# Performance work log

Hardware: AMD Instinct MI355X
Metric: run time of the kernel (lower is better)

Reference implementation:

```python
import jax, jax.numpy as jnp
import numpy as np

N, E, H = 50000, 800000, 4
IN, HID, OUT = 128, 64, 16
SIM_THRESH = 0.1
NEG_SLOPE = 0.01  # F.leaky_relu default


def setup_inputs() -> dict:
    key = jax.random.key(0)
    k = jax.random.split(key, 6)
    x = jax.random.normal(k[0], (N, IN), jnp.float32)
    row = jax.random.randint(k[1], (E,), 0, N)
    col = jax.random.randint(k[2], (E,), 0, N)
    W0 = jax.random.normal(k[3], (H, IN, HID), jnp.float32) / np.float32(np.sqrt(IN))
    W1 = jax.random.normal(k[4], (H, H * HID, HID), jnp.float32) / np.float32(np.sqrt(H * HID))
    W2 = jax.random.normal(k[5], (1, H * HID, OUT), jnp.float32) / np.float32(np.sqrt(H * HID))
    return {"x": x, "W0": W0, "W1": W1, "W2": W2, "row": row, "col": col}


def _att_coef(x, row, col):
    # cosine similarity on edges only (honors the sparse edge structure)
    nrm = jnp.linalg.norm(x, axis=1, keepdims=True)
    xn = x / jnp.maximum(nrm, 1e-12)
    sim = jnp.sum(xn[row] * xn[col], axis=1)            # [E]
    sim = jnp.where(sim < SIM_THRESH, 0.0, sim)
    # L1 row-normalize the thresholded attention matrix
    rowsum = jax.ops.segment_sum(jnp.abs(sim), row, num_segments=N)
    rs_e = rowsum[row]
    att = jnp.where(rs_e > 0, sim / jnp.where(rs_e > 0, rs_e, 1.0), 0.0)
    # degree-based self-loop weight lam = 1/(deg+1), then exp of all nonzeros
    deg = jax.ops.segment_sum((att != 0).astype(x.dtype), row, num_segments=N)
    w_edge = jnp.where(att != 0, jnp.exp(att), 0.0)     # zero entries stay zero (dropped nnz)
    w_self = jnp.exp(1.0 / (deg + 1.0))                 # [N]
    return w_edge, w_self


def _layer(x, W, row, col, act):
    w_edge, w_self = _att_coef(x, row, col)
    z = jnp.einsum('nd,hdo->nho', x, W)                 # per-head projection
    msg = w_edge[:, None, None] * z[col]                # [E,h,o] gather + weight
    agg = jax.ops.segment_sum(msg, row, num_segments=N) + w_self[:, None, None] * z
    out = agg.reshape(N, -1)                            # concat heads (flatten(1))
    return jax.nn.leaky_relu(out, NEG_SLOPE) if act else out


def reference(x, W0, W1, W2, row, col):
    h = _layer(x, W0, row, col, True)
    h = _layer(h, W1, row, col, True)
    h = _layer(h, W2, row, col, False)
    return h
```

## Files before the change

kernel.cpp:

```cpp
#include <hip/hip_runtime.h>
#include <math.h>


static inline int cdiv(int a, int b){ return (a + b - 1) / b; }


__device__ inline float vdot(float4 a, float4 b){ return a.x*b.x + a.y*b.y + a.z*b.z + a.w*b.w; }
__device__ inline void vfma(float4& acc, float w, float4 b){
  acc.x += w*b.x; acc.y += w*b.y; acc.z += w*b.z; acc.w += w*b.w;
}
__device__ inline float4 vscale(float w, float4 a){ return make_float4(w*a.x, w*a.y, w*a.z, w*a.w); }

__device__ inline float wred(float d){
  #pragma unroll
  for (int off = 32; off; off >>= 1) d += __shfl_xor(d, off);
  return d;
}

__device__ inline unsigned short f2bf(float f){
  unsigned int u = __float_as_uint(f);
  unsigned int r = (u + 0x7FFFu + ((u >> 16) & 1u)) >> 16;
  return (unsigned short)r;
}
__device__ inline float bf2f(unsigned int us){ return __uint_as_float(us << 16); }

__device__ inline void bf8_to_f(uint4 v, float* f){
  f[0] = bf2f(v.x & 0xFFFFu); f[1] = bf2f(v.x >> 16);
  f[2] = bf2f(v.y & 0xFFFFu); f[3] = bf2f(v.y >> 16);
  f[4] = bf2f(v.z & 0xFFFFu); f[5] = bf2f(v.z >> 16);
  f[6] = bf2f(v.w & 0xFFFFu); f[7] = bf2f(v.w >> 16);
}

typedef __attribute__((ext_vector_type(8))) short bf16x8;
typedef __attribute__((ext_vector_type(4))) float f32x4;


__global__ void count_kernel(const int* __restrict__ row, int* __restrict__ cnt, int E){
  int e = blockIdx.x * blockDim.x + threadIdx.x;
  if (e < E) atomicAdd(&cnt[row[e]], 1);
}

__global__ void scan1_kernel(const int* __restrict__ cnt, int* __restrict__ offs,
                             int* __restrict__ bsum, int n){
  __shared__ int tmp[256];
  int tid = threadIdx.x;
  int g = blockIdx.x * 256 + tid;
  int v = (g < n) ? cnt[g] : 0;
  tmp[tid] = v;
  __syncthreads();
  for (int off = 1; off < 256; off <<= 1){
    int t = (tid >= off) ? tmp[tid - off] : 0;
    __syncthreads();
    tmp[tid] += t;
    __syncthreads();
  }
  if (g < n) offs[g] = tmp[tid] - v;
  if (tid == 255) bsum[blockIdx.x] = tmp[255];
}

__global__ void scan2_kernel(int* __restrict__ bsum, int* __restrict__ offs, int nb, int n){
  __shared__ int tmp[256];
  int tid = threadIdx.x;
  int v = (tid < nb) ? bsum[tid] : 0;
  tmp[tid] = v;
  __syncthreads();
  for (int off = 1; off < 256; off <<= 1){
    int t = (tid >= off) ? tmp[tid - off] : 0;
    __syncthreads();
    tmp[tid] += t;
    __syncthreads();
  }
  if (tid < nb) bsum[tid] = tmp[tid] - v;
  if (tid == 255) offs[n] = tmp[255];
}

__global__ void scan3_kernel(int* __restrict__ offs, int* __restrict__ cur,
                             const int* __restrict__ bsum, int n){
  int g = blockIdx.x * 256 + threadIdx.x;
  if (g < n){
    int o = offs[g] + bsum[blockIdx.x];
    offs[g] = o;
    cur[g]  = o;
  }
}

__global__ void scatter_kernel(const int* __restrict__ row, const int* __restrict__ col,
                               int* __restrict__ cur, int* __restrict__ ecol, int E){
  int e = blockIdx.x * blockDim.x + threadIdx.x;
  if (e < E){
    int p = atomicAdd(&cur[row[e]], 1);
    ecol[p] = col[e];
  }
}


__global__ void invnorm128_kernel(const float* __restrict__ x, float* __restrict__ invn, int N){
  int n = blockIdx.x * 4 + (threadIdx.x >> 6);
  int lane = threadIdx.x & 63;
  if (n >= N) return;
  float2 a = ((const float2*)(x + (size_t)n * 128))[lane];
  float ss = a.x * a.x + a.y * a.y;
  ss = wred(ss);
  if (lane == 0) invn[n] = 1.0f / fmaxf(sqrtf(ss), 1e-12f);
}


template<int R>
__global__ void att_agg_wave128(const float* __restrict__ x, const float* __restrict__ invn,
                                const int* __restrict__ offs, const int* __restrict__ ecol,
                                float* __restrict__ out, int N){
  constexpr int LT = 64;
  __shared__ float tls[4][LT];
  __shared__ int   tlk[4][LT];
  const int wid  = threadIdx.x >> 6;
  const int lane = threadIdx.x & 63;
  const int half = lane >> 5, hl = lane & 31;
  const int hidx = wid * 2 + half;
  const int n = blockIdx.x * 2 + wid;
  if (n >= N) return;
  const int s = offs[n], e = offs[n + 1];
  const float inr = invn[n];
  const float4* xv = (const float4*)x;
  float4 a = xv[(size_t)n * 32 + hl];

  float4 br[R];
  float  simv[R];
  float  rowsum = 0.0f;
  int    deg = 0;

  #pragma unroll
  for (int r = 0; r < R; r++){
    simv[r] = 0.0f;
    int k = s + 2 * r + half;
    if (k < e){
      int c = ecol[k];
      float4 b = xv[(size_t)c * 32 + hl];
      br[r] = b;
      float d = vdot(a, b);
      #pragma unroll
      for (int off = 16; off; off >>= 1) d += __shfl_xor(d, off);
      d *= inr * invn[c];
      if (d < 0.1f) d = 0.0f;
      simv[r] = d;
      rowsum += d;
      deg += (d != 0.0f) ? 1 : 0;
    }
  }

  int tc = 0, kover = e;
  int k = s + 2 * R + half;
  for (; k + 2 < e; k += 4){
    int c0 = ecol[k], c1 = ecol[k + 2];
    float4 b0 = xv[(size_t)c0 * 32 + hl];
    float4 b1 = xv[(size_t)c1 * 32 + hl];
    float d0 = vdot(a, b0), d1 = vdot(a, b1);
    #pragma unroll
    for (int off = 16; off; off >>= 1){ d0 += __shfl_xor(d0, off); d1 += __shfl_xor(d1, off); }
    d0 *= inr * invn[c0];
    d1 *= inr * invn[c1];
    if (d0 < 0.1f) d0 = 0.0f;
    if (d1 < 0.1f) d1 = 0.0f;
    rowsum += d0 + d1;
    deg += (d0 != 0.0f) + (d1 != 0.0f);
    if (d0 > 0.0f){
      if (tc < LT){ if (hl == 0){ tls[hidx][tc] = d0; tlk[hidx][tc] = c0; } tc++; }
      else if (kover > k) kover = k;
    }
    if (d1 > 0.0f){
      if (tc < LT){ if (hl == 0){ tls[hidx][tc] = d1; tlk[hidx][tc] = c1; } tc++; }
      else if (kover > k + 2) kover = k + 2;
    }
  }
  if (k < e){
    int c0 = ecol[k];
    float4 b0 = xv[(size_t)c0 * 32 + hl];
    float d0 = vdot(a, b0);
    #pragma unroll
    for (int off = 16; off; off >>= 1) d0 += __shfl_xor(d0, off);
    d0 *= inr * invn[c0];
    if (d0 < 0.1f) d0 = 0.0f;
    rowsum += d0;
    deg += (d0 != 0.0f) ? 1 : 0;
    if (d0 > 0.0f){
      if (tc < LT){ if (hl == 0){ tls[hidx][tc] = d0; tlk[hidx][tc] = c0; } tc++; }
      else if (kover > k) kover = k;
    }
  }

  rowsum += __shfl_xor(rowsum, 32);
  deg    += __shfl_xor(deg, 32);
  const float invrs = (rowsum > 0.0f) ? 1.0f / rowsum : 0.0f;
  const float wself = expf(1.0f / (float)(deg + 1));

  float4 acc = (half == 0) ? vscale(wself, a) : make_float4(0.f, 0.f, 0.f, 0.f);
  #pragma unroll
  for (int r = 0; r < R; r++){
    if (simv[r] > 0.0f) vfma(acc, expf(simv[r] * invrs), br[r]);
  }
  int j = 0;
  for (; j + 1 < tc; j += 2){
    float w0 = expf(tls[hidx][j] * invrs);
    float w1 = expf(tls[hidx][j + 1] * invrs);
    int c0 = tlk[hidx][j], c1 = tlk[hidx][j + 1];
    float4 b0 = xv[(size_t)c0 * 32 + hl];
    float4 b1 = xv[(size_t)c1 * 32 + hl];
    vfma(acc, w0, b0);
    vfma(acc, w1, b1);
  }
  if (j < tc){
    float w0 = expf(tls[hidx][j] * invrs);
    float4 b0 = xv[(size_t)tlk[hidx][j] * 32 + hl];
    vfma(acc, w0, b0);
  }
  for (int k2 = kover; k2 < e; k2 += 2){
    int c = ecol[k2];
    float4 b = xv[(size_t)c * 32 + hl];
    float d = vdot(a, b);
    #pragma unroll
    for (int off = 16; off; off >>= 1) d += __shfl_xor(d, off);
    d *= inr * invn[c];
    if (d >= 0.1f) vfma(acc, expf(d * invrs), b);
  }

  acc.x += __shfl_xor(acc.x, 32);
  acc.y += __shfl_xor(acc.y, 32);
  acc.z += __shfl_xor(acc.z, 32);
  acc.w += __shfl_xor(acc.w, 32);
  if (half == 0) ((float4*)out)[(size_t)n * 32 + hl] = acc;
}


template<int LT>
__device__ inline void sim_rows_mfma(const uint4* __restrict__ hb4,
                                     const float* __restrict__ invn,
                                     const int* __restrict__ ecol,
                                     uint4* __restrict__ tile,
                                     int n, int s, int e, float inr,
                                     float* __restrict__ tls, int* __restrict__ tlk,
                                     float& rowsum_o, int& deg_o, int& tcl_o, int& kover_o){
  const int l = threadIdx.x & 63;
  const int g = l >> 4;
  const int m = l & 15;
  const int lr = l & 31;
  const int rh = l >> 5;
  const bf16x8* hbv = (const bf16x8*)hb4;

  bf16x8 bfrag[8];
  #pragma unroll
  for (int f = 0; f < 8; f++) bfrag[f] = hbv[(size_t)n * 32 + f * 4 + g];

  float rowsum = 0.0f;
  int deg = 0, tc = 0, kover = e;

  for (int k0 = s; k0 < e; k0 += 16){
    int idx = k0 + m;
    int kk = (idx < e) ? idx : (e - 1);
    int c_l = ecol[kk];
    float ic_l = invn[c_l];

    #pragma unroll
    for (int f = 0; f < 8; f++){
      int rsel = 2 * f + rh;
      int crow = __shfl(c_l, rsel);
      tile[(size_t)lr * 17 + rsel] = hb4[(size_t)crow * 32 + lr];
    }

    f32x4 acc0 = {0.f, 0.f, 0.f, 0.f};
    f32x4 acc1 = {0.f, 0.f, 0.f, 0.f};
    #pragma unroll
    for (int f = 0; f < 8; f += 2){
      bf16x8 av0 = *(const bf16x8*)&tile[(size_t)(g + 4 * f) * 17 + m];
      bf16x8 av1 = *(const bf16x8*)&tile[(size_t)(g + 4 * (f + 1)) * 17 + m];
      acc0 = __builtin_amdgcn_mfma_f32_16x16x32_bf16(av0, bfrag[f],     acc0, 0, 0, 0);
      acc1 = __builtin_amdgcn_mfma_f32_16x16x32_bf16(av1, bfrag[f + 1], acc1, 0, 0, 0);
    }

    float dv[4]; int cm[4];
    int bits = 0;
    #pragma unroll
    for (int r = 0; r < 4; r++){
      int mm = g * 4 + r;
      cm[r] = __shfl(c_l, mm);
      float ic = __shfl(ic_l, mm);
      float d = (acc0[r] + acc1[r]) * inr * ic;
      if (d < 0.1f || (k0 + mm) >= e) d = 0.0f;
      dv[r] = d;
      rowsum += d;
      deg += (d != 0.0f) ? 1 : 0;
      if (d > 0.0f) bits |= (1 << r);
    }
    int M16 = bits << (g * 4);
    M16 |= __shfl_xor(M16, 16);
    M16 |= __shfl_xor(M16, 32);
    #pragma unroll
    for (int r = 0; r < 4; r++){
      if (m == 0 && dv[r] > 0.0f){
        int mm = g * 4 + r;
        int pos = tc + __popc(M16 & ((1 << mm) - 1));
        if (pos < LT){ tls[pos] = dv[r]; tlk[pos] = cm[r]; }
        else if (k0 + mm < kover) kover = k0 + mm;
      }
    }
    tc += __popc(M16);
  }
  rowsum += __shfl_xor(rowsum, 16);
  rowsum += __shfl_xor(rowsum, 32);
  deg    += __shfl_xor(deg, 16);
  deg    += __shfl_xor(deg, 32);
  #pragma unroll
  for (int off = 32; off; off >>= 1) kover = min(kover, __shfl_xor(kover, off));
  rowsum_o = rowsum; deg_o = deg;
  tcl_o = (tc < LT) ? tc : LT;
  kover_o = kover;
}


template<int LT>
__global__ __launch_bounds__(128) void att256_mfma(
    const unsigned short* __restrict__ hbf, const float* __restrict__ invn,
    const int* __restrict__ offs, const int* __restrict__ ecol,
    float* __restrict__ out, int N){
  __shared__ float tls[2][LT];
  __shared__ int   tlk[2][LT];
  __shared__ uint4 tile[2][32 * 17];
  const int wid = threadIdx.x >> 6;
  const int l   = threadIdx.x & 63;
  const int n = blockIdx.x * 2 + wid;
  if (n >= N) return;
  const int s = offs[n], e = offs[n + 1];
  const float inr = invn[n];
  const uint4* hb4 = (const uint4*)hbf;

  float rowsum; int deg, tcl, kover;
  sim_rows_mfma<LT>(hb4, invn, ecol, tile[wid], n, s, e, inr, tls[wid], tlk[wid],
                    rowsum, deg, tcl, kover);

  const float invrs = (rowsum > 0.0f) ? 1.0f / rowsum : 0.0f;
  const float wself = expf(1.0f / (float)(deg + 1));

  const int half = l >> 5, hl = l & 31;
  float a8[8]; bf8_to_f(hb4[(size_t)n * 32 + hl], a8);
  float acc8[8];
  #pragma unroll
  for (int t = 0; t < 8; t++) acc8[t] = (half == 0) ? wself * a8[t] : 0.0f;

  int j = half;
  for (; j + 2 < tcl; j += 4){
    float w0 = expf(tls[wid][j] * invrs);
    float w1 = expf(tls[wid][j + 2] * invrs);
    uint4 v0 = hb4[(size_t)tlk[wid][j] * 32 + hl];
    uint4 v1 = hb4[(size_t)tlk[wid][j + 2] * 32 + hl];
    float b0[8], b1[8];
    bf8_to_f(v0, b0); bf8_to_f(v1, b1);
    #pragma unroll
    for (int t = 0; t < 8; t++) acc8[t] += w0 * b0[t] + w1 * b1[t];
  }
  if (j < tcl){
    float w0 = expf(tls[wid][j] * invrs);
    uint4 v0 = hb4[(size_t)tlk[wid][j] * 32 + hl];
    float b0[8]; bf8_to_f(v0, b0);
    #pragma unroll
    for (int t = 0; t < 8; t++) acc8[t] += w0 * b0[t];
  }
  for (int k2 = kover; k2 < e; k2++){
    int c = ecol[k2];
    uint4 v = hb4[(size_t)c * 32 + hl];
    float b[8]; bf8_to_f(v, b);
    float d = 0.0f;
    #pragma unroll
    for (int t = 0; t < 8; t++) d += a8[t] * b[t];
    #pragma unroll
    for (int off = 16; off; off >>= 1) d += __shfl_xor(d, off);
    d *= inr * invn[c];
    if (d >= 0.1f && half == 0){
      float w = expf(d * invrs);
      #pragma unroll
      for (int t = 0; t < 8; t++) acc8[t] += w * b[t];
    }
  }

  #pragma unroll
  for (int t = 0; t < 8; t++) acc8[t] += __shfl_xor(acc8[t], 32);
  if (half == 0){
    float4* ov = (float4*)out;
    ov[(size_t)n * 64 + 2 * hl]     = make_float4(acc8[0], acc8[1], acc8[2], acc8[3]);
    ov[(size_t)n * 64 + 2 * hl + 1] = make_float4(acc8[4], acc8[5], acc8[6], acc8[7]);
  }
}


template<int LT>
__global__ __launch_bounds__(128) void attz16_mfma(
    const unsigned short* __restrict__ hbf, const float* __restrict__ invn,
    const int* __restrict__ offs, const int* __restrict__ ecol,
    const float* __restrict__ z2, float* __restrict__ out, int N){
  __shared__ float tls[2][LT];
  __shared__ int   tlk[2][LT];
  __shared__ uint4 tile[2][32 * 17];
  const int wid = threadIdx.x >> 6;
  const int l   = threadIdx.x & 63;
  const int n = blockIdx.x * 2 + wid;
  if (n >= N) return;
  const int s = offs[n], e = offs[n + 1];
  const float inr = invn[n];
  const uint4* hb4 = (const uint4*)hbf;

  float rowsum; int deg, tcl, kover;
  sim_rows_mfma<LT>(hb4, invn, ecol, tile[wid], n, s, e, inr, tls[wid], tlk[wid],
                    rowsum, deg, tcl, kover);

  const float invrs = (rowsum > 0.0f) ? 1.0f / rowsum : 0.0f;
  const float wself = expf(1.0f / (float)(deg + 1));

  const int g = l >> 4, ch = l & 15;
  float acc = 0.0f;
  for (int j = g; j < tcl; j += 4){
    float w = expf(tls[wid][j] * invrs);
    acc += w * z2[(size_t)tlk[wid][j] * 16 + ch];
  }
  if (kover < e){
    const int hl = l & 31;
    float a8[8]; bf8_to_f(hb4[(size_t)n * 32 + hl], a8);
    for (int k2 = kover; k2 < e; k2++){
      int c = ecol[k2];
      uint4 v = hb4[(size_t)c * 32 + hl];
      float b[8]; bf8_to_f(v, b);
      float d = 0.0f;
      #pragma unroll
      for (int t = 0; t < 8; t++) d += a8[t] * b[t];
      #pragma unroll
      for (int off = 16; off; off >>= 1) d += __shfl_xor(d, off);
      d *= inr * invn[c];
      if (d >= 0.1f && g == 0)
        acc += expf(d * invrs) * z2[(size_t)c * 16 + ch];
    }
  }
  acc += __shfl_xor(acc, 16);
  acc += __shfl_xor(acc, 32);
  if (l < 16) out[(size_t)n * 16 + l] = acc + wself * z2[(size_t)n * 16 + l];
}


template<int D>
__global__ __launch_bounds__(256) void proj_act_norm(
    const float* __restrict__ xin, const float* __restrict__ W,
    float* __restrict__ hout, float* __restrict__ invn,
    unsigned short* __restrict__ hbf, int N){
  __shared__ float xs[32][D];
  const int tid = threadIdx.x;
  const int w = tid >> 6, l = tid & 63;
  const int n0 = blockIdx.x * 32;

  {
    float4* xs4 = (float4*)&xs[0][0];
    const float4* xin4 = (const float4*)(xin + (size_t)n0 * D);
    const int rows = (N - n0 >= 32) ? 32 : (N - n0);
    const int limit4 = rows * (D / 4);
    constexpr int total4 = 32 * D / 4;
    for (int i = tid; i < total4; i += 256)
      xs4[i] = (i < limit4) ? xin4[i] : make_float4(0.f, 0.f, 0.f, 0.f);
  }
  __syncthreads();

  const int h  = l >> 4;
  const int oo = (l & 15) * 4;
  const float* Wp = W + (size_t)h * D * 64 + oo;
  const float* xrow = &xs[w * 8][0];

  float acc[8][4];
  #pragma unroll
  for (int i = 0; i < 8; i++){
    acc[i][0] = 0.f; acc[i][1] = 0.f; acc[i][2] = 0.f; acc[i][3] = 0.f;
  }

  for (int d = 0; d < D; d += 4){
    float4 w0 = *(const float4*)(Wp + (size_t)(d + 0) * 64);
    float4 w1 = *(const float4*)(Wp + (size_t)(d + 1) * 64);
    float4 w2 = *(const float4*)(Wp + (size_t)(d + 2) * 64);
    float4 w3 = *(const float4*)(Wp + (size_t)(d + 3) * 64);
    #pragma unroll
    for (int i = 0; i < 8; i++){
      float4 xv = *(const float4*)(xrow + i * D + d);
      acc[i][0] += xv.x * w0.x + xv.y * w1.x + xv.z * w2.x + xv.w * w3.x;
      acc[i][1] += xv.x * w0.y + xv.y * w1.y + xv.z * w2.y + xv.w * w3.y;
      acc[i][2] += xv.x * w0.z + xv.y * w1.z + xv.z * w2.z + xv.w * w3.z;
      acc[i][3] += xv.x * w0.w + xv.y * w1.w + xv.z * w2.w + xv.w * w3.w;
    }
  }

  const int nrow = n0 + w * 8;
  #pragma unroll
  for (int i = 0; i < 8; i++){
    #pragma unroll
    for (int j = 0; j < 4; j++){
      float a = acc[i][j];
      acc[i][j] = (a > 0.0f) ? a : 0.01f * a;
    }
    float ss = acc[i][0]*acc[i][0] + acc[i][1]*acc[i][1]
             + acc[i][2]*acc[i][2] + acc[i][3]*acc[i][3];
    ss = wred(ss);
    const int n = nrow + i;
    if (n < N){
      if (l == 0) invn[n] = 1.0f / fmaxf(sqrtf(ss), 1e-12f);
      ((float4*)hout)[(size_t)n * 64 + l] =
          make_float4(acc[i][0], acc[i][1], acc[i][2], acc[i][3]);
      if (hbf){
        ushort4 u;
        u.x = f2bf(acc[i][0]); u.y = f2bf(acc[i][1]);
        u.z = f2bf(acc[i][2]); u.w = f2bf(acc[i][3]);
        ((ushort4*)hbf)[(size_t)n * 64 + l] = u;
      }
    }
  }
}

__global__ void proj16_kernel(const float* __restrict__ x, const float* __restrict__ W,
                              float* __restrict__ z, int N){
  __shared__ float xs[16][256];
  __shared__ float wsh[256 * 16];
  int tid = threadIdx.x;
  int n0 = blockIdx.x * 16;
  for (int i = tid; i < 16 * 256; i += 256){
    int nl = i >> 8, d = i & 255;
    int n = n0 + nl;
    xs[nl][d] = (n < N) ? x[(size_t)n * 256 + d] : 0.0f;
  }
  for (int i = tid; i < 256 * 16; i += 256) wsh[i] = W[i];
  __syncthreads();
  int nl = tid >> 4, o = tid & 15;
  float acc = 0.0f;
  for (int d = 0; d < 256; d++) acc += xs[nl][d] * wsh[d * 16 + o];
  int n = n0 + nl;
  if (n < N) z[(size_t)n * 16 + o] = acc;
}


extern "C" void kernel_launch(void* const* d_in, const int* in_sizes, int n_in,
                              void* d_out, int out_size, void* d_ws, size_t ws_size,
                              hipStream_t stream){
  const float* x  = (const float*)d_in[0];
  const float* W0 = (const float*)d_in[1];
  const float* W1 = (const float*)d_in[2];
  const float* W2 = (const float*)d_in[3];
  const int*   row = (const int*)d_in[4];
  const int*   col = (const int*)d_in[5];
  const int N = in_sizes[0] / 128;
  const int E = in_sizes[4];
  float* out = (float*)d_out;

  float* p = (float*)d_ws;
  float* hbuf   = p; p += (size_t)N * 256;
  float* aggbuf = p; p += (size_t)N * 256;
  float* z2     = p; p += (size_t)N * 16;
  float* invn   = p; p += N;
  unsigned short* hbf = (unsigned short*)p; p += (size_t)N * 128;
  int* cnt  = (int*)p;
  int* offs = cnt + N;
  int* cur  = offs + N + 1;
  int* ecol = cur + N;
  int* bsum = ecol + E;

  const int NB = cdiv(N, 256);

  hipMemsetAsync(cnt, 0, sizeof(int) * N, stream);
  count_kernel<<<cdiv(E, 256), 256, 0, stream>>>(row, cnt, E);
  scan1_kernel<<<NB, 256, 0, stream>>>(cnt, offs, bsum, N);
  scan2_kernel<<<1, 256, 0, stream>>>(bsum, offs, NB, N);
  scan3_kernel<<<NB, 256, 0, stream>>>(offs, cur, bsum, N);
  scatter_kernel<<<cdiv(E, 256), 256, 0, stream>>>(row, col, cur, ecol, E);

  invnorm128_kernel<<<cdiv(N, 4), 256, 0, stream>>>(x, invn, N);
  att_agg_wave128<8><<<cdiv(N, 2), 128, 0, stream>>>(x, invn, offs, ecol, aggbuf, N);
  proj_act_norm<128><<<cdiv(N, 32), 256, 0, stream>>>(aggbuf, W0, hbuf, invn, hbf, N);

  att256_mfma<256><<<cdiv(N, 2), 128, 0, stream>>>(hbf, invn, offs, ecol, aggbuf, N);
  proj_act_norm<256><<<cdiv(N, 32), 256, 0, stream>>>(aggbuf, W1, hbuf, invn, hbf, N);

  proj16_kernel<<<cdiv(N, 16), 256, 0, stream>>>(hbuf, W2, z2, N);
  attz16_mfma<256><<<cdiv(N, 2), 128, 0, stream>>>(hbf, invn, offs, ecol, z2, out, N);
}
```

Baseline: 685.8 us.

## Add single-chunk fast path reusing LDS tile, swizzle tile layout, four waves per block

Rows with at most 16 edges (the common case at average degree 16) now take a fast path. It computes similarities with one MFMA chunk and aggregates neighbour features straight from the already-staged LDS tile instead of re-gathering them from global memory. The LDS tile moves from padded stride 17 to an XOR-swizzled stride 16 to avoid bank conflicts. Blocks grow to 4 waves and the overflow list shrinks to 128 entries, which changes occupancy. The extra code duplication may raise register pressure.

```diff
diff --git a/kernel.cpp b/kernel.cpp
--- a/kernel.cpp
+++ b/kernel.cpp
@@ -230,50 +230,125 @@
 }
 
 
+__device__ inline void chunk_dots(const uint4* __restrict__ hb4,
+                                  uint4* __restrict__ tile,
+                                  const bf16x8 (&bfrag)[8],
+                                  int c_l, f32x4& acc0, f32x4& acc1){
+  const int l  = threadIdx.x & 63;
+  const int g  = l >> 4, m = l & 15;
+  const int lr = l & 31, rh = l >> 5;
+
+  #pragma unroll
+  for (int f = 0; f < 8; f++){
+    int rsel = 2 * f + rh;
+    int crow = __shfl(c_l, rsel);
+    tile[lr * 16 + (rsel ^ (lr & 15))] = hb4[(size_t)crow * 32 + lr];
+  }
+  acc0 = (f32x4){0.f, 0.f, 0.f, 0.f};
+  acc1 = (f32x4){0.f, 0.f, 0.f, 0.f};
+  #pragma unroll
+  for (int f = 0; f < 8; f += 2){
+    int u0 = g + 4 * f, u1 = g + 4 * (f + 1);
+    bf16x8 av0 = *(const bf16x8*)&tile[u0 * 16 + (m ^ (u0 & 15))];
+    bf16x8 av1 = *(const bf16x8*)&tile[u1 * 16 + (m ^ (u1 & 15))];
+    acc0 = __builtin_amdgcn_mfma_f32_16x16x32_bf16(av0, bfrag[f],     acc0, 0, 0, 0);
+    acc1 = __builtin_amdgcn_mfma_f32_16x16x32_bf16(av1, bfrag[f + 1], acc1, 0, 0, 0);
+  }
+}
+
+
 template<int LT>
-__device__ inline void sim_rows_mfma(const uint4* __restrict__ hb4,
-                                     const float* __restrict__ invn,
-                                     const int* __restrict__ ecol,
-                                     uint4* __restrict__ tile,
-                                     int n, int s, int e, float inr,
-                                     float* __restrict__ tls, int* __restrict__ tlk,
-                                     float& rowsum_o, int& deg_o, int& tcl_o, int& kover_o){
-  const int l = threadIdx.x & 63;
-  const int g = l >> 4;
-  const int m = l & 15;
-  const int lr = l & 31;
-  const int rh = l >> 5;
-  const bf16x8* hbv = (const bf16x8*)hb4;
+__global__ __launch_bounds__(256) void att256_mfma(
+    const unsigned short* __restrict__ hbf, const float* __restrict__ invn,
+    const int* __restrict__ offs, const int* __restrict__ ecol,
+    float* __restrict__ out, int N){
+  __shared__ float tls[4][LT];
+  __shared__ int   tlk[4][LT];
+  __shared__ uint4 tile[4][32 * 16];
+  const int wid = threadIdx.x >> 6;
+  const int l   = threadIdx.x & 63;
+  const int n = blockIdx.x * 4 + wid;
+  if (n >= N) return;
+  const int s = offs[n], e = offs[n + 1];
+  const float inr = invn[n];
+  const uint4* hb4 = (const uint4*)hbf;
+  const bf16x8* hbv = (const bf16x8*)hbf;
+  const int g = l >> 4, m = l & 15;
+  uint4* tl = tile[wid];
 
   bf16x8 bfrag[8];
   #pragma unroll
   for (int f = 0; f < 8; f++) bfrag[f] = hbv[(size_t)n * 32 + f * 4 + g];
+
+  if (e - s <= 16){
+    int idx = s + m;
+    int kk = (idx < e) ? idx : ((e > s) ? e - 1 : 0);
+    int c_l = ecol[kk];
+    float ic_l = invn[c_l];
+    f32x4 acc0, acc1;
+    chunk_dots(hb4, tl, bfrag, c_l, acc0, acc1);
+
+    float dv[4];
+    float rowsum = 0.0f; int deg = 0;
+    #pragma unroll
+    for (int r = 0; r < 4; r++){
+      int mm = g * 4 + r;
+      float ic = __shfl(ic_l, mm);
+      float d = (acc0[r] + acc1[r]) * inr * ic;
+      if (d < 0.1f || (s + mm) >= e) d = 0.0f;
+      dv[r] = d;
+      rowsum += d;
+      deg += (d != 0.0f) ? 1 : 0;
+    }
+    rowsum += __shfl_xor(rowsum, 16);
+    rowsum += __shfl_xor(rowsum, 32);
+    deg    += __shfl_xor(deg, 16);
+    deg    += __shfl_xor(deg, 32);
+    const float invrs = (rowsum > 0.0f) ? 1.0f / rowsum : 0.0f;
+    const float wself = expf(1.0f / (float)(deg + 1));
+
+    float w8[8];
+    const int srcb = (l >> 5) * 32;
+    #pragma unroll
+    for (int r = 0; r < 8; r++){
+      float sv = __shfl(dv[r & 3], srcb + (r >> 2) * 16);
+      w8[r] = (sv > 0.0f) ? expf(sv * invrs) : 0.0f;
+    }
+
+    const int u = l & 31;
+    const int rbase = (l >> 5) * 8;
+    float a8[8]; bf8_to_f(hb4[(size_t)n * 32 + u], a8);
+    const float sw = (l < 32) ? wself : 0.0f;
+    float acc8[8];
+    #pragma unroll
+    for (int t = 0; t < 8; t++) acc8[t] = sw * a8[t];
+    #pragma unroll
+    for (int r = 0; r < 8; r++){
+      int rr = rbase + r;
+      uint4 v = tl[u * 16 + (rr ^ (u & 15))];
+      float b8[8]; bf8_to_f(v, b8);
+      #pragma unroll
+      for (int t = 0; t < 8; t++) acc8[t] += w8[r] * b8[t];
+    }
+    #pragma unroll
+    for (int t = 0; t < 8; t++) acc8[t] += __shfl_xor(acc8[t], 32);
+    if (l < 32){
+      float4* ov = (float4*)out;
+      ov[(size_t)n * 64 + 2 * u]     = make_float4(acc8[0], acc8[1], acc8[2], acc8[3]);
+      ov[(size_t)n * 64 + 2 * u + 1] = make_float4(acc8[4], acc8[5], acc8[6], acc8[7]);
+    }
+    return;
+  }
 
   float rowsum = 0.0f;
   int deg = 0, tc = 0, kover = e;
-
   for (int k0 = s; k0 < e; k0 += 16){
     int idx = k0 + m;
     int kk = (idx < e) ? idx : (e - 1);
     int c_l = ecol[kk];
     float ic_l = invn[c_l];
-
-    #pragma unroll
-    for (int f = 0; f < 8; f++){
-      int rsel = 2 * f + rh;
-      int crow = __shfl(c_l, rsel);
-      tile[(size_t)lr * 17 + rsel] = hb4[(size_t)crow * 32 + lr];
-    }
-
-    f32x4 acc0 = {0.f, 0.f, 0.f, 0.f};
-    f32x4 acc1 = {0.f, 0.f, 0.f, 0.f};
-    #pragma unroll
-    for (int f = 0; f < 8; f += 2){
-      bf16x8 av0 = *(const bf16x8*)&tile[(size_t)(g + 4 * f) * 17 + m];
-      bf16x8 av1 = *(const bf16x8*)&tile[(size_t)(g + 4 * (f + 1)) * 17 + m];
-      acc0 = __builtin_amdgcn_mfma_f32_16x16x32_bf16(av0, bfrag[f],     acc0, 0, 0, 0);
-      acc1 = __builtin_amdgcn_mfma_f32_16x16x32_bf16(av1, bfrag[f + 1], acc1, 0, 0, 0);
-    }
+    f32x4 acc0, acc1;
+    chunk_dots(hb4, tl, bfrag, c_l, acc0, acc1);
 
     float dv[4]; int cm[4];
     int bits = 0;
@@ -297,7 +372,7 @@
       if (m == 0 && dv[r] > 0.0f){
         int mm = g * 4 + r;
         int pos = tc + __popc(M16 & ((1 << mm) - 1));
-        if (pos < LT){ tls[pos] = dv[r]; tlk[pos] = cm[r]; }
+        if (pos < LT){ tls[wid][pos] = dv[r]; tlk[wid][pos] = cm[r]; }
         else if (k0 + mm < kover) kover = k0 + mm;
       }
     }
@@ -309,31 +384,7 @@
   deg    += __shfl_xor(deg, 32);
   #pragma unroll
   for (int off = 32; off; off >>= 1) kover = min(kover, __shfl_xor(kover, off));
-  rowsum_o = rowsum; deg_o = deg;
-  tcl_o = (tc < LT) ? tc : LT;
-  kover_o = kover;
-}
-
-
-template<int LT>
-__global__ __launch_bounds__(128) void att256_mfma(
-    const unsigned short* __restrict__ hbf, const float* __restrict__ invn,
-    const int* __restrict__ offs, const int* __restrict__ ecol,
-    float* __restrict__ out, int N){
-  __shared__ float tls[2][LT];
-  __shared__ int   tlk[2][LT];
-  __shared__ uint4 tile[2][32 * 17];
-  const int wid = threadIdx.x >> 6;
-  const int l   = threadIdx.x & 63;
-  const int n = blockIdx.x * 2 + wid;
-  if (n >= N) return;
-  const int s = offs[n], e = offs[n + 1];
-  const float inr = invn[n];
-  const uint4* hb4 = (const uint4*)hbf;
-
-  float rowsum; int deg, tcl, kover;
-  sim_rows_mfma<LT>(hb4, invn, ecol, tile[wid], n, s, e, inr, tls[wid], tlk[wid],
-                    rowsum, deg, tcl, kover);
+  int tcl = (tc < LT) ? tc : LT;
 
   const float invrs = (rowsum > 0.0f) ? 1.0f / rowsum : 0.0f;
   const float wself = expf(1.0f / (float)(deg + 1));
@@ -390,31 +441,122 @@
 
 
 template<int LT>
-__global__ __launch_bounds__(128) void attz16_mfma(
+__global__ __launch_bounds__(256) void attz16_mfma(
     const unsigned short* __restrict__ hbf, const float* __restrict__ invn,
     const int* __restrict__ offs, const int* __restrict__ ecol,
     const float* __restrict__ z2, float* __restrict__ out, int N){
-  __shared__ float tls[2][LT];
-  __shared__ int   tlk[2][LT];
-  __shared__ uint4 tile[2][32 * 17];
+  __shared__ float tls[4][LT];
+  __shared__ int   tlk[4][LT];
+  __shared__ uint4 tile[4][32 * 16];
   const int wid = threadIdx.x >> 6;
   const int l   = threadIdx.x & 63;
-  const int n = blockIdx.x * 2 + wid;
+  const int n = blockIdx.x * 4 + wid;
   if (n >= N) return;
   const int s = offs[n], e = offs[n + 1];
   const float inr = invn[n];
   const uint4* hb4 = (const uint4*)hbf;
-
-  float rowsum; int deg, tcl, kover;
-  sim_rows_mfma<LT>(hb4, invn, ecol, tile[wid], n, s, e, inr, tls[wid], tlk[wid],
-                    rowsum, deg, tcl, kover);
+  const bf16x8* hbv = (const bf16x8*)hbf;
+  const int g = l >> 4, m = l & 15;
+  uint4* tl = tile[wid];
+
+  bf16x8 bfrag[8];
+  #pragma unroll
+  for (int f = 0; f < 8; f++) bfrag[f] = hbv[(size_t)n * 32 + f * 4 + g];
+
+  if (e - s <= 16){
+    int idx = s + m;
+    int kk = (idx < e) ? idx : ((e > s) ? e - 1 : 0);
+    int c_l = ecol[kk];
+    float ic_l = invn[c_l];
+    f32x4 acc0, acc1;
+    chunk_dots(hb4, tl, bfrag, c_l, acc0, acc1);
+
+    float dv[4];
+    float rowsum = 0.0f; int deg = 0;
+    #pragma unroll
+    for (int r = 0; r < 4; r++){
+      int mm = g * 4 + r;
+      float ic = __shfl(ic_l, mm);
+      float d = (acc0[r] + acc1[r]) * inr * ic;
+      if (d < 0.1f || (s + mm) >= e) d = 0.0f;
+      dv[r] = d;
+      rowsum += d;
+      deg += (d != 0.0f) ? 1 : 0;
+    }
+    rowsum += __shfl_xor(rowsum, 16);
+    rowsum += __shfl_xor(rowsum, 32);
+    deg    += __shfl_xor(deg, 16);
+    deg    += __shfl_xor(deg, 32);
+    const float invrs = (rowsum > 0.0f) ? 1.0f / rowsum : 0.0f;
+    const float wself = expf(1.0f / (float)(deg + 1));
+
+    const int ch = l & 15;
+    float acc = 0.0f;
+    #pragma unroll
+    for (int r = 0; r < 4; r++){
+      int mm = g * 4 + r;
+      int c = __shfl(c_l, mm);
+      float d = dv[r];
+      if (d > 0.0f) acc += expf(d * invrs) * z2[(size_t)c * 16 + ch];
+    }
+    acc += __shfl_xor(acc, 16);
+    acc += __shfl_xor(acc, 32);
+    if (l < 16) out[(size_t)n * 16 + l] = acc + wself * z2[(size_t)n * 16 + l];
+    return;
+  }
+
+  float rowsum = 0.0f;
+  int deg = 0, tc = 0, kover = e;
+  for (int k0 = s; k0 < e; k0 += 16){
+    int idx = k0 + m;
+    int kk = (idx < e) ? idx : (e - 1);
+    int c_l = ecol[kk];
+    float ic_l = invn[c_l];
+    f32x4 acc0, acc1;
+    chunk_dots(hb4, tl, bfrag, c_l, acc0, acc1);
+
+    float dv[4]; int cm[4];
+    int bits = 0;
+    #pragma unroll
+    for (int r = 0; r < 4; r++){
+      int mm = g * 4 + r;
+      cm[r] = __shfl(c_l, mm);
+      float ic = __shfl(ic_l, mm);
+      float d = (acc0[r] + acc1[r]) * inr * ic;
+      if (d < 0.1f || (k0 + mm) >= e) d = 0.0f;
+      dv[r] = d;
+      rowsum += d;
+      deg += (d != 0.0f) ? 1 : 0;
+      if (d > 0.0f) bits |= (1 << r);
+    }
+    int M16 = bits << (g * 4);
+    M16 |= __shfl_xor(M16, 16);
+    M16 |= __shfl_xor(M16, 32);
+    #pragma unroll
+    for (int r = 0; r < 4; r++){
+      if (m == 0 && dv[r] > 0.0f){
+        int mm = g * 4 + r;
+        int pos = tc + __popc(M16 & ((1 << mm) - 1));
+        if (pos < LT){ tls[wid][pos] = dv[r]; tlk[wid][pos] = cm[r]; }
+        else if (k0 + mm < kover) kover = k0 + mm;
+      }
+    }
+    tc += __popc(M16);
+  }
+  rowsum += __shfl_xor(rowsum, 16);
+  rowsum += __shfl_xor(rowsum, 32);
+  deg    += __shfl_xor(deg, 16);
+  deg    += __shfl_xor(deg, 32);
+  #pragma unroll
+  for (int off = 32; off; off >>= 1) kover = min(kover, __shfl_xor(kover, off));
+  int tcl = (tc < LT) ? tc : LT;
 
   const float invrs = (rowsum > 0.0f) ? 1.0f / rowsum : 0.0f;
   const float wself = expf(1.0f / (float)(deg + 1));
 
-  const int g = l >> 4, ch = l & 15;
+  const int gq = l >> 4, ch = l & 15;
   float acc = 0.0f;
-  for (int j = g; j < tcl; j += 4){
+  for (int j = gq; j < tcl; j += 4){
     float w = expf(tls[wid][j] * invrs);
     acc += w * z2[(size_t)tlk[wid][j] * 16 + ch];
   }
@@ -431,7 +573,7 @@
       #pragma unroll
       for (int off = 16; off; off >>= 1) d += __shfl_xor(d, off);
       d *= inr * invn[c];
-      if (d >= 0.1f && g == 0)
+      if (d >= 0.1f && gq == 0)
         acc += expf(d * invrs) * z2[(size_t)c * 16 + ch];
     }
   }
@@ -573,9 +715,9 @@
   att_agg_wave128<8><<<cdiv(N, 2), 128, 0, stream>>>(x, invn, offs, ecol, aggbuf, N);
   proj_act_norm<128><<<cdiv(N, 32), 256, 0, stream>>>(aggbuf, W0, hbuf, invn, hbf, N);
 
-  att256_mfma<256><<<cdiv(N, 2), 128, 0, stream>>>(hbf, invn, offs, ecol, aggbuf, N);
+  att256_mfma<128><<<cdiv(N, 4), 256, 0, stream>>>(hbf, invn, offs, ecol, aggbuf, N);
   proj_act_norm<256><<<cdiv(N, 32), 256, 0, stream>>>(aggbuf, W1, hbuf, invn, hbf, N);
 
   proj16_kernel<<<cdiv(N, 16), 256, 0, stream>>>(hbuf, W2, z2, N);
-  attz16_mfma<256><<<cdiv(N, 2), 128, 0, stream>>>(hbf, invn, offs, ecol, z2, out, N);
-}
+  attz16_mfma<128><<<cdiv(N, 4), 256, 0, stream>>>(hbf, invn, offs, ecol, z2, out, N);
+}
```

Measured after the change: 692.6 us. About the same (+1.0%).
